# Kernel tuning notes

Hardware: AMD Instinct MI355X
Metric: run time of the kernel (lower is better)

The kernel has to match this reference:

```python
import jax, jax.numpy as jnp
import numpy as np

B, CIN, COUT, K, H, W = 8, 512, 512, 3, 64, 64
SCALE = 1.0 / np.sqrt(CIN * K * K).astype(np.float32)  # conv.scale
LRELU_SCALE = 1.4142135623730951  # sqrt(2), FusedLeakyReLU scale


def setup_inputs() -> dict:
    key = jax.random.key(0)
    ks = jax.random.split(key, 6)
    return {
        "x": jax.random.normal(ks[0], (B, CIN, H, W), jnp.float32),
        "style": jax.random.normal(ks[1], (B, CIN), jnp.float32),
        "noise": jax.random.normal(ks[2], (1, 1, H, W), jnp.float32),
        "weight": jax.random.normal(ks[3], (COUT, CIN, K, K), jnp.float32),
        "bias": jnp.zeros((COUT,), jnp.float32),
        "noise_strength": jax.random.uniform(ks[4], (1,), jnp.float32),
    }


def reference(x, style, noise, weight, bias, noise_strength):
    # Modulate: scale * weight * style  -> [B, Cout, Cin, K, K]
    w = SCALE * weight[None] * style[:, None, :, None, None]
    # Demodulate per (batch, out_channel)
    demod = jax.lax.rsqrt(jnp.sum(w * w, axis=(2, 3, 4)) + 1e-8)
    w = w * demod[:, :, None, None, None]
    # Per-sample conv (grouped-conv trick in torch) via vmap over batch
    pad = K // 2
    def conv_one(xi, wi):  # xi: [Cin,H,W], wi: [Cout,Cin,K,K]
        return jax.lax.conv_general_dilated(
            xi[None], wi, window_strides=(1, 1),
            padding=[(pad, pad), (pad, pad)],
            dimension_numbers=("NCHW", "OIHW", "NCHW"))[0]
    out = jax.vmap(conv_one)(x, w)  # [B, Cout, H, W]
    # NoiseInjection: out + strength * noise (noise broadcast over B, C)
    out = out + noise_strength[0] * noise
    # FusedLeakyReLU: leaky_relu(out + bias, 0.2) * sqrt(2)
    y = out + bias[None, :, None, None]
    return jnp.where(y >= 0, y, 0.2 * y) * LRELU_SCALE
```

## Files before the change

kernel.cpp:

```cpp
#include <hip/hip_runtime.h>
#include <hip/hip_bf16.h>

typedef __attribute__((ext_vector_type(8))) short s16x8;
typedef __attribute__((ext_vector_type(4))) float f32x4;

#define MOD_SCALE 0.014731391274719739f

__device__ __forceinline__ void gload_lds16(const void* g, void* l) {
    __builtin_amdgcn_global_load_lds(
        (const __attribute__((address_space(1))) unsigned int*)g,
        (__attribute__((address_space(3))) unsigned int*)l, 16, 0, 0);
}

__global__ __launch_bounds__(256) void k_prep(const float* __restrict__ x,
                                              const float* __restrict__ style,
                                              const float* __restrict__ weight,
                                              __hip_bfloat16* __restrict__ xs,
                                              __hip_bfloat16* __restrict__ wb,
                                              float* __restrict__ dem) {
    __shared__ __align__(16) char sm[16896];
    const int t = threadIdx.x;
    const int bid = blockIdx.x;

    if (bid < 520) {
        const int idx = bid * 256 + t;
        const int b = idx / 16640;
        const int r2 = idx - b * 16640;
        const int pair = r2 >> 6;
        const int ciq = r2 & 63;
        int pr, pc;
        if (pair < 66)       { pr = 0;          pc = pair; }
        else if (pair < 132) { pr = 65;         pc = pair - 66; }
        else if (pair < 196) { pr = pair - 131; pc = 0; }
        else                 { pr = pair - 195; pc = 65; }
        uint4* d = (uint4*)(xs + (((size_t)b * 66 + pr) * 66 + pc) * 512) + ciq;
        *d = make_uint4(0u, 0u, 0u, 0u);
    } else if (bid < 2568) {
        const int r = bid - 520;
        const int cig = r & 3, h = (r >> 2) & 63, b = r >> 8;
        const int ci0 = cig * 128;
        __hip_bfloat16 (*tile)[130] = (__hip_bfloat16(*)[130])sm;
        const int wl = t & 63, cl4 = t >> 6;
        for (int rr = 0; rr < 32; ++rr) {
            int c = rr * 4 + cl4;
            float v = x[(((size_t)b * 512 + ci0 + c) * 64 + h) * 64 + wl];
            float s = style[b * 512 + ci0 + c];
            tile[wl][c] = __float2bfloat16(v * s * MOD_SCALE);
        }
        __syncthreads();
        const int w4 = t >> 6;
        const int cp = (t & 63) * 2;
        for (int rr = 0; rr < 16; ++rr) {
            int w = rr * 4 + w4;
            unsigned v = *(const unsigned*)(&tile[w][cp]);
            *(unsigned*)(&xs[(((size_t)b * 66 + h + 1) * 66 + (w + 1)) * 512 +
                             ci0 + cp]) = v;
        }
    } else if (bid < 3592) {
        const int r = bid - 2568;
        float* lds = (float*)sm;
        const int p0 = r * 256;
        const float* src = weight + (size_t)p0 * 9;
#pragma unroll
        for (int k = 0; k < 9; ++k) lds[k * 256 + t] = src[k * 256 + t];
        __syncthreads();
#pragma unroll
        for (int tap = 0; tap < 9; ++tap)
            wb[(size_t)tap * 262144 + p0 + t] = __float2bfloat16(lds[t * 9 + tap]);
    } else {
        const int co = bid - 3592;
        float* s2 = (float*)sm;
        for (int i = t; i < 4096; i += 256) { float v = style[i]; s2[i] = v * v; }
        __syncthreads();
        const float4* wp = (const float4*)(weight + (size_t)co * 4608);
        float acc[8] = {0.f, 0.f, 0.f, 0.f, 0.f, 0.f, 0.f, 0.f};
        for (int j = t; j < 1152; j += 256) {
            float4 v = wp[j];
            float w2[4] = {v.x * v.x, v.y * v.y, v.z * v.z, v.w * v.w};
            int base = j * 4;
#pragma unroll
            for (int e = 0; e < 4; ++e) {
                int ci = (base + e) / 9;
                float ww = w2[e];
#pragma unroll
                for (int bb = 0; bb < 8; ++bb) acc[bb] += ww * s2[bb * 512 + ci];
            }
        }
#pragma unroll
        for (int bb = 0; bb < 8; ++bb)
            for (int off = 32; off > 0; off >>= 1)
                acc[bb] += __shfl_down(acc[bb], off);
        float* red = (float*)(sm + 16384);
        const int wv = t >> 6, lane = t & 63;
        if (lane == 0) {
#pragma unroll
            for (int bb = 0; bb < 8; ++bb) red[wv * 8 + bb] = acc[bb];
        }
        __syncthreads();
        if (t < 8) {
            float s = red[t] + red[8 + t] + red[16 + t] + red[24 + t];
            const float S2 = MOD_SCALE * MOD_SCALE;
            dem[t * 512 + co] = rsqrtf(S2 * s + 1e-8f);
        }
    }
}

__global__ __launch_bounds__(256, 4) void k_conv(
    const __hip_bfloat16* __restrict__ xs,
    const __hip_bfloat16* __restrict__ wb,
    const float* __restrict__ demod,
    const float* __restrict__ noise,
    const float* __restrict__ bias,
    const float* __restrict__ nstr,
    float* __restrict__ out) {
    __shared__ __align__(16) char Xl[16896];
    __shared__ __align__(16) char Wl[2][8192];

    const int t = threadIdx.x;
    const int bi = blockIdx.x;
    const int spat = bi & 255;
    const int b = spat >> 5;
    const int h0 = (spat & 31) << 1;
    const int co0 = (bi >> 8) << 7;
    const int lane = t & 63;
    const int wv = t >> 6;
    const int wm = wv & 1, wn = wv >> 1;
    const int q = lane >> 4, ln = lane & 15;

    f32x4 acc[4][4];
#pragma unroll
    for (int i = 0; i < 4; ++i)
#pragma unroll
        for (int j = 0; j < 4; ++j) acc[i][j] = (f32x4){0.f, 0.f, 0.f, 0.f};

    const char* xsb = (const char*)xs + (size_t)b * 66 * 66 * 1024;
    const char* xsrc[4];
#pragma unroll
    for (int i = 0; i < 4; ++i) {
        int g = i * 256 + t;
        int e = g >> 2, s = g & 3;
        int r = e / 66, c = e - r * 66;
        int gc = s ^ (e & 3);
        xsrc[i] = xsb + (size_t)((h0 + r) * 66 + c) * 1024 + gc * 16;
    }
    const char* xsrct;
    {
        int e = 256 + (t >> 2), s = t & 3;
        int c = e - 198;
        int gc = s ^ (e & 3);
        xsrct = xsb + (size_t)((h0 + 3) * 66 + c) * 1024 + gc * 16;
    }
    const char* wsrcb[2];
#pragma unroll
    for (int i = 0; i < 2; ++i) {
        int g = i * 256 + t;
        int e = g >> 2, s = g & 3;
        int gc = s ^ (e & 3);
        wsrcb[i] = (const char*)wb + (size_t)(co0 + e) * 1024 + gc * 16;
    }
    char* ldsXw = Xl + (wv << 10);

#pragma unroll
    for (int i = 0; i < 4; ++i) gload_lds16(xsrc[i], ldsXw + i * 4096);
    if (t < 32) gload_lds16(xsrct, Xl + 16384);
#pragma unroll
    for (int i = 0; i < 2; ++i)
        gload_lds16(wsrcb[i], Wl[0] + (wv << 10) + i * 4096);
    __syncthreads();

    int g = 0;
    for (int cb = 0; cb < 16; ++cb) {
        const int cboff = cb * 64;
#pragma unroll
        for (int tap = 0; tap < 9; ++tap, ++g) {
            if (tap < 8) {
#pragma unroll
                for (int i = 0; i < 2; ++i)
                    gload_lds16(wsrcb[i] + (tap + 1) * 524288 + cboff,
                                Wl[(g + 1) & 1] + (wv << 10) + i * 4096);
            } else if (cb < 15) {
#pragma unroll
                for (int i = 0; i < 2; ++i)
                    gload_lds16(wsrcb[i] + cboff + 64,
                                Wl[(g + 1) & 1] + (wv << 10) + i * 4096);
            }
            const int dh = tap / 3, dw = tap % 3;
            const char* Wb = Wl[g & 1];
            s16x8 af[4], bfr[4];
            const char* abase = Wb + (wm * 64 + ln) * 64 + ((q ^ (ln & 3)) << 4);
#pragma unroll
            for (int mi = 0; mi < 4; ++mi)
                af[mi] = *(const s16x8*)(abase + mi * 1024);
            const int ecol = (dh + wn) * 66 + dw + ln;
            const char* bbase = Xl + ecol * 64 + ((q ^ (ecol & 3)) << 4);
#pragma unroll
            for (int ni = 0; ni < 4; ++ni)
                bfr[ni] = *(const s16x8*)(bbase + ni * 1024);
#pragma unroll
            for (int mi = 0; mi < 4; ++mi)
#pragma unroll
                for (int ni = 0; ni < 4; ++ni)
                    acc[mi][ni] = __builtin_amdgcn_mfma_f32_16x16x32_bf16(
                        af[mi], bfr[ni], acc[mi][ni], 0, 0, 0);
            __syncthreads();
        }
        if (cb < 15) {
#pragma unroll
            for (int i = 0; i < 4; ++i)
                gload_lds16(xsrc[i] + cboff + 64, ldsXw + i * 4096);
            if (t < 32) gload_lds16(xsrct + cboff + 64, Xl + 16384);
            __syncthreads();
        }
    }

    const float nsv = nstr[0];
    const int h = h0 + wn;
    const float LR = 1.4142135623730951f;
#pragma unroll
    for (int mi = 0; mi < 4; ++mi) {
        float dm[4], bs[4];
#pragma unroll
        for (int r = 0; r < 4; ++r) {
            int co = co0 + wm * 64 + mi * 16 + q * 4 + r;
            dm[r] = demod[b * 512 + co];
            bs[r] = bias[co];
        }
#pragma unroll
        for (int ni = 0; ni < 4; ++ni) {
            int w = ni * 16 + ln;
            float nz = nsv * noise[h * 64 + w];
#pragma unroll
            for (int r = 0; r < 4; ++r) {
                int co = co0 + wm * 64 + mi * 16 + q * 4 + r;
                float v = acc[mi][ni][r] * dm[r] + nz + bs[r];
                v = (v >= 0.f ? v : 0.2f * v) * LR;
                out[(((size_t)b * 512 + co) * 64 + h) * 64 + w] = v;
            }
        }
    }
}

extern "C" void kernel_launch(void* const* d_in, const int* in_sizes, int n_in,
                              void* d_out, int out_size, void* d_ws, size_t ws_size,
                              hipStream_t stream) {
    const float* x      = (const float*)d_in[0];
    const float* style  = (const float*)d_in[1];
    const float* noise  = (const float*)d_in[2];
    const float* weight = (const float*)d_in[3];
    const float* bias   = (const float*)d_in[4];
    const float* nstr   = (const float*)d_in[5];
    float* out = (float*)d_out;

    char* ws = (char*)d_ws;
    __hip_bfloat16* xs = (__hip_bfloat16*)ws;
    __hip_bfloat16* wb = (__hip_bfloat16*)(ws + 35684352);
    float* demod = (float*)(ws + 35684352 + 4718592);

    k_prep<<<4104, 256, 0, stream>>>(x, style, weight, xs, wb, demod);
    k_conv<<<1024, 256, 0, stream>>>(xs, wb, demod, noise, bias, nstr, out);
}
```

Before: 270.0 us.

## Enlarge conv tile to four rows and switch to 32x32x16 MFMA

Each conv block now covers 128 output channels by 4 image rows instead of 2, which halves the grid and doubles how often each loaded weight tile is reused. The inner product moves from 16x16x32 to 32x32x16 bf16 MFMA with a rotation-based LDS swizzle in place of the XOR swizzle, and launch bounds drop to 2 blocks per CU to fit the larger accumulator set. An explicit wait on all outstanding memory operations is added before every barrier so async global-to-LDS loads are complete. The trade-off is fewer resident waves for latency hiding and a larger LDS input tile, in exchange for lower weight traffic and more work per MFMA issue.

```diff
diff --git a/kernel.cpp b/kernel.cpp
--- a/kernel.cpp
+++ b/kernel.cpp
@@ -2,7 +2,7 @@
 #include <hip/hip_bf16.h>
 
 typedef __attribute__((ext_vector_type(8))) short s16x8;
-typedef __attribute__((ext_vector_type(4))) float f32x4;
+typedef __attribute__((ext_vector_type(16))) float f32x16;
 
 #define MOD_SCALE 0.014731391274719739f
 
@@ -10,6 +10,11 @@
     __builtin_amdgcn_global_load_lds(
         (const __attribute__((address_space(1))) unsigned int*)g,
         (__attribute__((address_space(3))) unsigned int*)l, 16, 0, 0);
+}
+
+__device__ __forceinline__ void sync_drain() {
+    __builtin_amdgcn_s_waitcnt(0);
+    __syncthreads();
 }
 
 __global__ __launch_bounds__(256) void k_prep(const float* __restrict__ x,
@@ -105,7 +110,7 @@
     }
 }
 
-__global__ __launch_bounds__(256, 4) void k_conv(
+__global__ __launch_bounds__(256, 2) void k_conv(
     const __hip_bfloat16* __restrict__ xs,
     const __hip_bfloat16* __restrict__ wb,
     const float* __restrict__ demod,
@@ -113,60 +118,63 @@
     const float* __restrict__ bias,
     const float* __restrict__ nstr,
     float* __restrict__ out) {
-    __shared__ __align__(16) char Xl[16896];
+    __shared__ __align__(16) char Xl[25344];
     __shared__ __align__(16) char Wl[2][8192];
 
     const int t = threadIdx.x;
     const int bi = blockIdx.x;
-    const int spat = bi & 255;
-    const int b = spat >> 5;
-    const int h0 = (spat & 31) << 1;
-    const int co0 = (bi >> 8) << 7;
+    const int spat = bi & 127;
+    const int b = spat >> 4;
+    const int h0 = (spat & 15) << 2;
+    const int co0 = (bi >> 7) << 7;
     const int lane = t & 63;
     const int wv = t >> 6;
     const int wm = wv & 1, wn = wv >> 1;
-    const int q = lane >> 4, ln = lane & 15;
-
-    f32x4 acc[4][4];
-#pragma unroll
-    for (int i = 0; i < 4; ++i)
-#pragma unroll
-        for (int j = 0; j < 4; ++j) acc[i][j] = (f32x4){0.f, 0.f, 0.f, 0.f};
+    const int el = lane & 31;
+    const int hk = lane >> 5;
+
+    f32x16 acc[2][4];
+#pragma unroll
+    for (int i = 0; i < 2; ++i)
+#pragma unroll
+        for (int j = 0; j < 4; ++j)
+#pragma unroll
+            for (int k = 0; k < 16; ++k) acc[i][j][k] = 0.f;
 
     const char* xsb = (const char*)xs + (size_t)b * 66 * 66 * 1024;
-    const char* xsrc[4];
-#pragma unroll
-    for (int i = 0; i < 4; ++i) {
+    const char* xsrc[7];
+#pragma unroll
+    for (int i = 0; i < 6; ++i) {
         int g = i * 256 + t;
         int e = g >> 2, s = g & 3;
-        int r = e / 66, c = e - r * 66;
-        int gc = s ^ (e & 3);
-        xsrc[i] = xsb + (size_t)((h0 + r) * 66 + c) * 1024 + gc * 16;
-    }
-    const char* xsrct;
+        int gc = (s - (e >> 2)) & 3;
+        int row = e / 66, col = e - row * 66;
+        xsrc[i] = xsb + (size_t)((h0 + row) * 66 + col) * 1024 + gc * 16;
+    }
     {
-        int e = 256 + (t >> 2), s = t & 3;
-        int c = e - 198;
-        int gc = s ^ (e & 3);
-        xsrct = xsb + (size_t)((h0 + 3) * 66 + c) * 1024 + gc * 16;
-    }
-    const char* wsrcb[2];
+        int g = 1536 + t;
+        int e = g >> 2, s = g & 3;
+        int gc = (s - (e >> 2)) & 3;
+        int row = e / 66, col = e - row * 66;
+        xsrc[6] = xsb + (size_t)((h0 + row) * 66 + col) * 1024 + gc * 16;
+    }
+    const char* wsrc[2];
 #pragma unroll
     for (int i = 0; i < 2; ++i) {
         int g = i * 256 + t;
         int e = g >> 2, s = g & 3;
-        int gc = s ^ (e & 3);
-        wsrcb[i] = (const char*)wb + (size_t)(co0 + e) * 1024 + gc * 16;
-    }
-    char* ldsXw = Xl + (wv << 10);
-
-#pragma unroll
-    for (int i = 0; i < 4; ++i) gload_lds16(xsrc[i], ldsXw + i * 4096);
-    if (t < 32) gload_lds16(xsrct, Xl + 16384);
+        int gc = (s - (e >> 2)) & 3;
+        wsrc[i] = (const char*)wb + (size_t)(co0 + e) * 1024 + gc * 16;
+    }
+    const int wvoff = wv << 10;
+
+#pragma unroll
+    for (int i = 0; i < 6; ++i) gload_lds16(xsrc[i], Xl + i * 4096 + wvoff);
+    if (t < 48) gload_lds16(xsrc[6], Xl + 24576);
 #pragma unroll
     for (int i = 0; i < 2; ++i)
-        gload_lds16(wsrcb[i], Wl[0] + (wv << 10) + i * 4096);
-    __syncthreads();
+        gload_lds16(wsrc[i], Wl[0] + i * 4096 + wvoff);
+    sync_drain();
 
     int g = 0;
     for (int cb = 0; cb < 16; ++cb) {
@@ -174,65 +182,75 @@
 #pragma unroll
         for (int tap = 0; tap < 9; ++tap, ++g) {
             if (tap < 8) {
+                char* Wn = Wl[(g + 1) & 1] + wvoff;
 #pragma unroll
                 for (int i = 0; i < 2; ++i)
-                    gload_lds16(wsrcb[i] + (tap + 1) * 524288 + cboff,
-                                Wl[(g + 1) & 1] + (wv << 10) + i * 4096);
+                    gload_lds16(wsrc[i] + (size_t)(tap + 1) * 524288 + cboff,
+                                Wn + i * 4096);
             } else if (cb < 15) {
+                char* Wn = Wl[(g + 1) & 1] + wvoff;
 #pragma unroll
                 for (int i = 0; i < 2; ++i)
-                    gload_lds16(wsrcb[i] + cboff + 64,
-                                Wl[(g + 1) & 1] + (wv << 10) + i * 4096);
+                    gload_lds16(wsrc[i] + cboff + 64, Wn + i * 4096);
             }
             const int dh = tap / 3, dw = tap % 3;
             const char* Wb = Wl[g & 1];
-            s16x8 af[4], bfr[4];
-            const char* abase = Wb + (wm * 64 + ln) * 64 + ((q ^ (ln & 3)) << 4);
-#pragma unroll
-            for (int mi = 0; mi < 4; ++mi)
-                af[mi] = *(const s16x8*)(abase + mi * 1024);
-            const int ecol = (dh + wn) * 66 + dw + ln;
-            const char* bbase = Xl + ecol * 64 + ((q ^ (ecol & 3)) << 4);
-#pragma unroll
-            for (int ni = 0; ni < 4; ++ni)
-                bfr[ni] = *(const s16x8*)(bbase + ni * 1024);
-#pragma unroll
-            for (int mi = 0; mi < 4; ++mi)
-#pragma unroll
-                for (int ni = 0; ni < 4; ++ni)
-                    acc[mi][ni] = __builtin_amdgcn_mfma_f32_16x16x32_bf16(
-                        af[mi], bfr[ni], acc[mi][ni], 0, 0, 0);
-            __syncthreads();
+#pragma unroll
+            for (int ks = 0; ks < 2; ++ks) {
+                const int c = 2 * ks + hk;
+                s16x8 af[2], bfr[4];
+#pragma unroll
+                for (int mi = 0; mi < 2; ++mi) {
+                    int e = wm * 64 + mi * 32 + el;
+                    af[mi] = *(const s16x8*)(Wb + e * 64 +
+                                             (((c + (e >> 2)) & 3) << 4));
+                }
+#pragma unroll
+                for (int ni = 0; ni < 4; ++ni) {
+                    int e = (2 * wn + (ni >> 1) + dh) * 66 + dw +
+                            (ni & 1) * 32 + el;
+                    bfr[ni] = *(const s16x8*)(Xl + e * 64 +
+                                              (((c + (e >> 2)) & 3) << 4));
+                }
+#pragma unroll
+                for (int mi = 0; mi < 2; ++mi)
+#pragma unroll
+                    for (int ni = 0; ni < 4; ++ni)
+                        acc[mi][ni] = __builtin_amdgcn_mfma_f32_32x32x16_bf16(
+                            af[mi], bfr[ni], acc[mi][ni], 0, 0, 0);
+            }
+            sync_drain();
         }
         if (cb < 15) {
 #pragma unroll
-            for (int i = 0; i < 4; ++i)
-                gload_lds16(xsrc[i] + cboff + 64, ldsXw + i * 4096);
-            if (t < 32) gload_lds16(xsrct + cboff + 64, Xl + 16384);
-            __syncthreads();
+            for (int i = 0; i < 6; ++i)
+                gload_lds16(xsrc[i] + cboff + 64, Xl + i * 4096 + wvoff);
+            if (t < 48) gload_lds16(xsrc[6] + cboff + 64, Xl + 24576);
+            sync_drain();
         }
     }
 
     const float nsv = nstr[0];
-    const int h = h0 + wn;
     const float LR = 1.4142135623730951f;
 #pragma unroll
-    for (int mi = 0; mi < 4; ++mi) {
-        float dm[4], bs[4];
-#pragma unroll
-        for (int r = 0; r < 4; ++r) {
-            int co = co0 + wm * 64 + mi * 16 + q * 4 + r;
-            dm[r] = demod[b * 512 + co];
-            bs[r] = bias[co];
+    for (int mi = 0; mi < 2; ++mi) {
+        float dm[16], bs[16];
+#pragma unroll
+        for (int rg = 0; rg < 16; ++rg) {
+            int co = co0 + wm * 64 + mi * 32 + (rg & 3) + 8 * (rg >> 2) + 4 * hk;
+            dm[rg] = demod[b * 512 + co];
+            bs[rg] = bias[co];
         }
 #pragma unroll
         for (int ni = 0; ni < 4; ++ni) {
-            int w = ni * 16 + ln;
+            int h = h0 + 2 * wn + (ni >> 1);
+            int w = (ni & 1) * 32 + el;
             float nz = nsv * noise[h * 64 + w];
 #pragma unroll
-            for (int r = 0; r < 4; ++r) {
-                int co = co0 + wm * 64 + mi * 16 + q * 4 + r;
-                float v = acc[mi][ni][r] * dm[r] + nz + bs[r];
+            for (int rg = 0; rg < 16; ++rg) {
+                int co = co0 + wm * 64 + mi * 32 + (rg & 3) + 8 * (rg >> 2) +
+                         4 * hk;
+                float v = acc[mi][ni][rg] * dm[rg] + nz + bs[rg];
                 v = (v >= 0.f ? v : 0.2f * v) * LR;
                 out[(((size_t)b * 512 + co) * 64 + h) * 64 + w] = v;
             }
@@ -257,5 +275,5 @@
     float* demod = (float*)(ws + 35684352 + 4718592);
 
     k_prep<<<4104, 256, 0, stream>>>(x, style, weight, xs, wb, demod);
-    k_conv<<<1024, 256, 0, stream>>>(xs, wb, demod, noise, bias, nstr, out);
-}
+    k_conv<<<512, 256, 0, stream>>>(xs, wb, demod, noise, bias, nstr, out);
+}
```

Measured after the change: 254.8 us. -5.7%, faster.
